# Kernel optimization log

Measured on AMD Instinct MI355X. Metric: run time of the kernel, lower is better.

The kernel has to match this reference:

```python
import jax, jax.numpy as jnp
import numpy as np

B, NQ, NK = 4, 512, 512
DQ, DK, DV = 512, 512, 512
H = 128
MASK_VAL = -1e6


def setup_inputs() -> dict:
    key = jax.random.key(0)
    kq, kk, kv, kwq, kwk, kwv, kl = jax.random.split(key, 7)
    queries = jax.random.normal(kq, (B, NQ, DQ), dtype=jnp.float32)
    keys = jax.random.normal(kk, (B, NK, DK), dtype=jnp.float32)
    values = jax.random.normal(kv, (B, NK, DV), dtype=jnp.float32)
    # Dense(num_hiddens, use_bias=False) weights, Glorot-ish scale
    Wq = jax.random.normal(kwq, (DQ, H), dtype=jnp.float32) / np.sqrt(DQ)
    Wk = jax.random.normal(kwk, (DK, H), dtype=jnp.float32) / np.sqrt(DK)
    Wv = jax.random.normal(kwv, (H,), dtype=jnp.float32) / np.sqrt(H)  # Dense(1) as a vector
    valid_lens = jax.random.randint(kl, (B,), 1, NK + 1, dtype=jnp.int32)
    return {"queries": queries, "keys": keys, "values": values,
            "Wq": Wq, "Wk": Wk, "Wv": Wv, "valid_lens": valid_lens}


def reference(queries, keys, values, Wq, Wk, Wv, valid_lens):
    # Project queries/keys to hidden dim
    q = jnp.einsum('bqd,dh->bqh', queries, Wq)   # [B,NQ,H]
    k = jnp.einsum('bkd,dh->bkh', keys, Wk)      # [B,NK,H]
    # Broadcast add + tanh -> [B,NQ,NK,H] (the big intermediate)
    features = jnp.tanh(q[:, :, None, :] + k[:, None, :, :])
    # W_v reduces hidden dim to a scalar score
    scores = jnp.einsum('bqkh,h->bqk', features, Wv)  # [B,NQ,NK]
    # masked softmax over keys: positions >= valid_len get -1e6 (as in d2l sequence_mask)
    mask = jnp.arange(NK, dtype=jnp.int32)[None, None, :] < valid_lens[:, None, None]
    scores = jnp.where(mask, scores, MASK_VAL)
    attn = jax.nn.softmax(scores, axis=-1)
    # dropout rate 0.0 -> identity
    return jnp.einsum('bqk,bkv->bqv', attn, values)  # [B,NQ,DV]
```

## Files before the change

### kernel.cpp

```cpp
#include <hip/hip_runtime.h>

#ifndef __has_builtin
#define __has_builtin(x) 0
#endif

#if __has_builtin(__builtin_amdgcn_exp2f)
#define EXP2F(x) __builtin_amdgcn_exp2f(x)
#else
#define EXP2F(x) exp2f(x)
#endif
#if __has_builtin(__builtin_amdgcn_rcpf)
#define RCPF(x) __builtin_amdgcn_rcpf(x)
#else
#define RCPF(x) (1.0f / (x))
#endif

static constexpr int NB = 4, NQ = 512, NK = 512, DD = 512, HH = 128, DV = 512;
static constexpr float MASKV = -1e6f;
static constexpr float C2LOG2E = 2.885390081777926814f;

typedef __attribute__((ext_vector_type(8))) short bf16x8;
typedef __attribute__((ext_vector_type(4))) float f32x4;

__device__ __forceinline__ unsigned short f2bf(float x) {
  unsigned int u = __float_as_uint(x);
  u += 0x7FFFu + ((u >> 16) & 1u);
  return (unsigned short)(u >> 16);
}
__device__ __forceinline__ float bf2f(unsigned short h) {
  return __uint_as_float(((unsigned int)h) << 16);
}
__device__ __forceinline__ void split2(float x, unsigned short& hi, unsigned short& lo) {
  hi = f2bf(x);
  lo = f2bf(x - bf2f(hi));
}

__global__ __launch_bounds__(256) void proj_mfma_vt_kernel(
    const float* __restrict__ queries, const float* __restrict__ keys,
    const float* __restrict__ Wq, const float* __restrict__ Wk,
    const float* __restrict__ values, const int* __restrict__ valid_lens,
    float* __restrict__ eq, float* __restrict__ ekT4,
    unsigned short* __restrict__ Vt) {
  __shared__ __align__(16) unsigned short smem_us[20736];
  const int bid = blockIdx.x;
  const int t = threadIdx.x;

  if (bid < 256) {
    const int row0 = bid << 4;
    const bool isK = row0 >= 2048;
    int b = 0, kloc = 0;
    const float* inb;
    const float* W;
    if (isK) {
      const int local = row0 - 2048;
      b = local >> 9;
      kloc = local & 511;
      if (kloc >= valid_lens[b]) return;
      inb = keys + (size_t)local * DD;
      W = Wk;
    } else {
      inb = queries + (size_t)row0 * DD;
      W = Wq;
    }

    unsigned short* Ah = smem_us;
    unsigned short* Al = smem_us + 1152;
    unsigned short* Wh = smem_us + 2304;
    unsigned short* Wl = smem_us + 11520;

    const int w = t >> 6, l = t & 63;
    const int lm = l & 15;
    const int lk8 = (l >> 4) << 3;

    const f32x4 z = {0.f, 0.f, 0.f, 0.f};
    f32x4 acc[2] = {z, z};

    const int ar = t >> 4, ac4 = (t & 15) << 2;
    const int wh = t & 127, wkg = (t >> 7) << 5;

    for (int kt = 0; kt < 8; ++kt) {
      const int k0 = kt << 6;
      {
        const float4 v = *reinterpret_cast<const float4*>(inb + (size_t)ar * DD + k0 + ac4);
        unsigned short h0, h1, h2, h3, l0, l1, l2, l3;
        split2(v.x, h0, l0); split2(v.y, h1, l1);
        split2(v.z, h2, l2); split2(v.w, h3, l3);
        uint2 ph = make_uint2((unsigned int)h0 | ((unsigned int)h1 << 16),
                              (unsigned int)h2 | ((unsigned int)h3 << 16));
        uint2 pl = make_uint2((unsigned int)l0 | ((unsigned int)l1 << 16),
                              (unsigned int)l2 | ((unsigned int)l3 << 16));
        *reinterpret_cast<uint2*>(Ah + ar * 72 + ac4) = ph;
        *reinterpret_cast<uint2*>(Al + ar * 72 + ac4) = pl;
      }
      {
        unsigned int hw[16], lw[16];
#pragma unroll
        for (int i = 0; i < 16; ++i) {
          const float w0 = W[(size_t)(k0 + wkg + 2 * i) * HH + wh];
          const float w1 = W[(size_t)(k0 + wkg + 2 * i + 1) * HH + wh];
          unsigned short a0, a1, b0, b1;
          split2(w0, a0, b0); split2(w1, a1, b1);
          hw[i] = (unsigned int)a0 | ((unsigned int)a1 << 16);
          lw[i] = (unsigned int)b0 | ((unsigned int)b1 << 16);
        }
        unsigned int* dh = reinterpret_cast<unsigned int*>(Wh + wh * 72 + wkg);
        unsigned int* dl = reinterpret_cast<unsigned int*>(Wl + wh * 72 + wkg);
#pragma unroll
        for (int i = 0; i < 4; ++i) {
          *reinterpret_cast<uint4*>(dh + 4 * i) =
              make_uint4(hw[4 * i], hw[4 * i + 1], hw[4 * i + 2], hw[4 * i + 3]);
          *reinterpret_cast<uint4*>(dl + 4 * i) =
              make_uint4(lw[4 * i], lw[4 * i + 1], lw[4 * i + 2], lw[4 * i + 3]);
        }
      }
      __syncthreads();

#pragma unroll
      for (int kh = 0; kh < 2; ++kh) {
        const int ko = lk8 + (kh << 5);
        const bf16x8 ah = *reinterpret_cast<const bf16x8*>(Ah + lm * 72 + ko);
        const bf16x8 al = *reinterpret_cast<const bf16x8*>(Al + lm * 72 + ko);
#pragma unroll
        for (int c = 0; c < 2; ++c) {
          const int hrow = (w << 5) + (c << 4) + lm;
          const bf16x8 bh = *reinterpret_cast<const bf16x8*>(Wh + hrow * 72 + ko);
          const bf16x8 bl = *reinterpret_cast<const bf16x8*>(Wl + hrow * 72 + ko);
          acc[c] = __builtin_amdgcn_mfma_f32_16x16x32_bf16(ah, bh, acc[c], 0, 0, 0);
          acc[c] = __builtin_amdgcn_mfma_f32_16x16x32_bf16(al, bh, acc[c], 0, 0, 0);
          acc[c] = __builtin_amdgcn_mfma_f32_16x16x32_bf16(ah, bl, acc[c], 0, 0, 0);
        }
      }
      __syncthreads();
    }

    const int rb = (l >> 4) << 2;
    if (!isK) {
#pragma unroll
      for (int c = 0; c < 2; ++c) {
        const int h = (w << 5) + (c << 4) + lm;
#pragma unroll
        for (int j = 0; j < 4; ++j)
          eq[(size_t)(row0 + rb + j) * HH + h] = EXP2F(acc[c][j] * C2LOG2E);
      }
    } else {
      float* tile = reinterpret_cast<float*>(smem_us);
#pragma unroll
      for (int c = 0; c < 2; ++c) {
        const int h = (w << 5) + (c << 4) + lm;
#pragma unroll
        for (int j = 0; j < 4; ++j)
          tile[(rb + j) * 132 + h] = EXP2F(acc[c][j] * C2LOG2E);
      }
      __syncthreads();
#pragma unroll
      for (int i = 0; i < 2; ++i) {
        const int idx = t + (i << 8);
        const int k = idx & 15, h4 = idx >> 4;
        const float4 v = *reinterpret_cast<const float4*>(tile + k * 132 + (h4 << 2));
        *reinterpret_cast<float4*>(
            ekT4 + ((((size_t)b * 32 + h4) << 9) + kloc + k) * 4) = v;
      }
    }
  } else {
    unsigned short (*tl)[72] = reinterpret_cast<unsigned short (*)[72]>(smem_us);
    const int vb = bid - 256;
    const int b = vb >> 6;
    const int tile = vb & 63;
    const int k0 = (tile >> 3) << 6;
    const int v0 = (tile & 7) << 6;
    const int kr = t >> 4, c4 = (t & 15) << 2;
#pragma unroll
    for (int pp = 0; pp < 4; ++pp) {
      const int k = kr + (pp << 4);
      const float4 v = *reinterpret_cast<const float4*>(
          values + ((size_t)(b * NK + k0 + k)) * DV + v0 + c4);
      tl[k][c4 + 0] = f2bf(v.x); tl[k][c4 + 1] = f2bf(v.y);
      tl[k][c4 + 2] = f2bf(v.z); tl[k][c4 + 3] = f2bf(v.w);
    }
    __syncthreads();
    const int vr = t >> 2, seg = t & 3;
    unsigned int pk[8];
#pragma unroll
    for (int i = 0; i < 8; ++i) {
      const int kc = (seg << 4) + (i << 1);
      pk[i] = (unsigned int)tl[kc][vr] | ((unsigned int)tl[kc + 1][vr] << 16);
    }
    unsigned short* dst = Vt + ((size_t)(b * NK + v0 + vr)) * NK + k0 + (seg << 4);
    *reinterpret_cast<uint4*>(dst) = make_uint4(pk[0], pk[1], pk[2], pk[3]);
    *reinterpret_cast<uint4*>(dst + 8) = make_uint4(pk[4], pk[5], pk[6], pk[7]);
  }
}

__global__ __launch_bounds__(1024) void scores_softmax_kernel(
    const float* __restrict__ eq, const float* __restrict__ ekT4,
    const float* __restrict__ Wv, const int* __restrict__ valid_lens,
    unsigned short* __restrict__ attnQ) {
  const int b = blockIdx.x >> 7;
  const int q0 = (blockIdx.x & 127) << 2;
  const int t = threadIdx.x;
  const int kk = t & 511, hh = t >> 9;

  __shared__ __align__(16) float qs[4][HH];
  __shared__ __align__(16) float wv[HH];
  __shared__ __align__(16) float scp[2][4][NK];

  if (t < 512) {
    qs[t >> 7][t & 127] = eq[((size_t)(b * NQ + q0 + (t >> 7))) * HH + (t & 127)];
  } else if (t < 640) {
    wv[t - 512] = Wv[t - 512];
  }
  __syncthreads();

  const int vl = valid_lens[b];
  float s0 = 0.f, s1 = 0.f, s2 = 0.f, s3 = 0.f;

  if (kk < vl) {
    const float* ekb4 = ekT4 + (((size_t)(b * 32 + hh * 16) << 9) + kk) * 4;
#pragma unroll 8
    for (int i = 0; i < 16; ++i) {
      const float4 e4 = *reinterpret_cast<const float4*>(ekb4 + ((size_t)i << 11));
      const int h = (hh * 16 + i) << 2;
      const float4 w4 = *reinterpret_cast<const float4*>(&wv[h]);
      const float4 qa = *reinterpret_cast<const float4*>(&qs[0][h]);
      const float4 qb = *reinterpret_cast<const float4*>(&qs[1][h]);
      const float4 qc = *reinterpret_cast<const float4*>(&qs[2][h]);
      const float4 qd = *reinterpret_cast<const float4*>(&qs[3][h]);
      float u, v, num, r;
      u = fmaf(qa.x, e4.x, 1.f); v = fmaf(qa.y, e4.y, 1.f);
      num = fmaf(w4.x, v, w4.y * u); r = RCPF(u * v); s0 = fmaf(num, r, s0);
      u = fmaf(qa.z, e4.z, 1.f); v = fmaf(qa.w, e4.w, 1.f);
      num = fmaf(w4.z, v, w4.w * u); r = RCPF(u * v); s0 = fmaf(num, r, s0);
      u = fmaf(qb.x, e4.x, 1.f); v = fmaf(qb.y, e4.y, 1.f);
      num = fmaf(w4.x, v, w4.y * u); r = RCPF(u * v); s1 = fmaf(num, r, s1);
      u = fmaf(qb.z, e4.z, 1.f); v = fmaf(qb.w, e4.w, 1.f);
      num = fmaf(w4.z, v, w4.w * u); r = RCPF(u * v); s1 = fmaf(num, r, s1);
      u = fmaf(qc.x, e4.x, 1.f); v = fmaf(qc.y, e4.y, 1.f);
      num = fmaf(w4.x, v, w4.y * u); r = RCPF(u * v); s2 = fmaf(num, r, s2);
      u = fmaf(qc.z, e4.z, 1.f); v = fmaf(qc.w, e4.w, 1.f);
      num = fmaf(w4.z, v, w4.w * u); r = RCPF(u * v); s2 = fmaf(num, r, s2);
      u = fmaf(qd.x, e4.x, 1.f); v = fmaf(qd.y, e4.y, 1.f);
      num = fmaf(w4.x, v, w4.y * u); r = RCPF(u * v); s3 = fmaf(num, r, s3);
      u = fmaf(qd.z, e4.z, 1.f); v = fmaf(qd.w, e4.w, 1.f);
      num = fmaf(w4.z, v, w4.w * u); r = RCPF(u * v); s3 = fmaf(num, r, s3);
    }
  }
  scp[hh][0][kk] = s0;
  scp[hh][1][kk] = s1;
  scp[hh][2][kk] = s2;
  scp[hh][3][kk] = s3;
  __syncthreads();

  if (t < 256) {
    const int w = t >> 6, l = t & 63;
    float v[8];
#pragma unroll
    for (int j = 0; j < 8; ++j) {
      const int k = l + (j << 6);
      const float sv = scp[0][w][k] + scp[1][w][k];
      v[j] = (k < vl) ? (-2.f * sv) : MASKV;
    }
    float m = v[0];
#pragma unroll
    for (int j = 1; j < 8; ++j) m = fmaxf(m, v[j]);
#pragma unroll
    for (int off = 32; off > 0; off >>= 1) m = fmaxf(m, __shfl_xor(m, off, 64));
    float p[8], sum = 0.f;
#pragma unroll
    for (int j = 0; j < 8; ++j) {
      p[j] = __expf(v[j] - m);
      sum += p[j];
    }
#pragma unroll
    for (int off = 32; off > 0; off >>= 1) sum += __shfl_xor(sum, off, 64);
    const float inv = RCPF(sum);
#pragma unroll
    for (int j = 0; j < 8; ++j) scp[0][w][l + (j << 6)] = p[j] * inv;
  }
  __syncthreads();

  if (t < 512) {
#pragma unroll
    for (int j = 0; j < 4; ++j)
      attnQ[((size_t)(b * NQ + q0 + j)) * NK + t] = f2bf(scp[0][j][t]);
  }
}

__global__ __launch_bounds__(256) void pv_mfma_kernel(
    const unsigned short* __restrict__ attnQ, const unsigned short* __restrict__ Vt,
    const int* __restrict__ valid_lens, float* __restrict__ out) {
  const int bid = blockIdx.x;
  const int b = (bid & 1) | ((bid >> 8) << 1);
  const int tile = (bid >> 1) & 127;
  const int q0 = (tile >> 4) << 6;
  const int v0 = (tile & 15) << 5;

  __shared__ __align__(16) unsigned short Als[64 * 40];
  __shared__ __align__(16) unsigned short Bls[32 * 40];

  const int t = threadIdx.x;
  const int w = t >> 6, l = t & 63;
  const int lm = l & 15;
  const int lk = (l >> 4) << 3;

  const f32x4 z = {0.f, 0.f, 0.f, 0.f};
  f32x4 acc[2] = {z, z};

  const int vl = valid_lens[b];
  const int nkt = (vl + 31) >> 5;

  const int sq = t >> 2, seg = t & 3;
  const unsigned short* arow = attnQ + ((size_t)(b * NQ + q0 + sq)) * NK;
  unsigned short* alds = &Als[sq * 40 + (seg << 3)];
  const unsigned short* brow = Vt + ((size_t)(b * NK + v0 + (t >> 2))) * NK;
  unsigned short* blds = &Bls[(t >> 2) * 40 + (seg << 3)];

  for (int kt = 0; kt < nkt; ++kt) {
    const int k0 = kt << 5;
    *reinterpret_cast<bf16x8*>(alds) =
        *reinterpret_cast<const bf16x8*>(arow + k0 + (seg << 3));
    if (t < 128)
      *reinterpret_cast<bf16x8*>(blds) =
          *reinterpret_cast<const bf16x8*>(brow + k0 + (seg << 3));
    __syncthreads();

    const bf16x8 af = *reinterpret_cast<const bf16x8*>(
        &Als[((w << 4) + lm) * 40 + lk]);
#pragma unroll
    for (int nv = 0; nv < 2; ++nv) {
      const bf16x8 bfr = *reinterpret_cast<const bf16x8*>(
          &Bls[((nv << 4) + lm) * 40 + lk]);
      acc[nv] = __builtin_amdgcn_mfma_f32_16x16x32_bf16(af, bfr, acc[nv], 0, 0, 0);
    }
    __syncthreads();
  }

  const int rbase = (l >> 4) << 2;
#pragma unroll
  for (int nv = 0; nv < 2; ++nv) {
    const int qg = q0 + (w << 4) + rbase;
    const int vg = v0 + (nv << 4) + lm;
#pragma unroll
    for (int j = 0; j < 4; ++j)
      out[((size_t)(b * NQ + qg + j)) * DV + vg] = acc[nv][j];
  }
}

extern "C" void kernel_launch(void* const* d_in, const int* in_sizes, int n_in,
                              void* d_out, int out_size, void* d_ws, size_t ws_size,
                              hipStream_t stream) {
  (void)in_sizes; (void)n_in; (void)out_size; (void)ws_size;
  const float* queries = (const float*)d_in[0];
  const float* keys    = (const float*)d_in[1];
  const float* values  = (const float*)d_in[2];
  const float* Wq      = (const float*)d_in[3];
  const float* Wk      = (const float*)d_in[4];
  const float* Wv      = (const float*)d_in[5];
  const int*   vlens   = (const int*)d_in[6];
  float* out = (float*)d_out;
  float* ws = (float*)d_ws;

  float* eq   = ws;
  float* ekT4 = ws + 262144;
  unsigned short* attnQ = (unsigned short*)(ws + 524288);
  unsigned short* Vt    = (unsigned short*)(ws + 1048576);

  proj_mfma_vt_kernel<<<512, 256, 0, stream>>>(queries, keys, Wq, Wk, values,
                                               vlens, eq, ekT4, Vt);
  scores_softmax_kernel<<<512, 1024, 0, stream>>>(eq, ekT4, Wv, vlens, attnQ);
  pv_mfma_kernel<<<512, 256, 0, stream>>>(attnQ, Vt, vlens, out);
}
```

Before: 44.87 us.

## Double-buffer PV kernel LDS tiles with larger 64x64 blocks and K=64 steps

Restructures the attention-times-V MFMA kernel so each block computes a 64x64 output tile with 512 threads, 8 waves arranged 4 in q by 2 in v. Each K step now covers 64 instead of 32. A double-buffered LDS scheme prefetches the next K slice into registers while MFMAs run on the current one, which cuts one barrier per iteration. The intent is to hide global load latency and raise data reuse per block. The trade-off is half as many blocks (256), which may reduce occupancy across CUs, and more LDS per block.

```diff
diff --git a/kernel.cpp b/kernel.cpp
--- a/kernel.cpp
+++ b/kernel.cpp
@@ -285,60 +285,84 @@
   }
 }
 
-__global__ __launch_bounds__(256) void pv_mfma_kernel(
+__global__ __launch_bounds__(512) void pv_mfma_kernel(
     const unsigned short* __restrict__ attnQ, const unsigned short* __restrict__ Vt,
     const int* __restrict__ valid_lens, float* __restrict__ out) {
   const int bid = blockIdx.x;
-  const int b = (bid & 1) | ((bid >> 8) << 1);
-  const int tile = (bid >> 1) & 127;
-  const int q0 = (tile >> 4) << 6;
-  const int v0 = (tile & 15) << 5;
-
-  __shared__ __align__(16) unsigned short Als[64 * 40];
-  __shared__ __align__(16) unsigned short Bls[32 * 40];
+  const int b = bid & 3;
+  const int tile = bid >> 2;
+  const int q0 = (tile >> 3) << 6;
+  const int v0 = (tile & 7) << 6;
+
+  __shared__ __align__(16) unsigned short Als[2][64 * 72];
+  __shared__ __align__(16) unsigned short Bls[2][64 * 72];
 
   const int t = threadIdx.x;
   const int w = t >> 6, l = t & 63;
   const int lm = l & 15;
   const int lk = (l >> 4) << 3;
+  const int wq = (w & 3) << 4;
+  const int wv = (w >> 2) << 5;
 
   const f32x4 z = {0.f, 0.f, 0.f, 0.f};
   f32x4 acc[2] = {z, z};
 
   const int vl = valid_lens[b];
-  const int nkt = (vl + 31) >> 5;
-
-  const int sq = t >> 2, seg = t & 3;
-  const unsigned short* arow = attnQ + ((size_t)(b * NQ + q0 + sq)) * NK;
-  unsigned short* alds = &Als[sq * 40 + (seg << 3)];
-  const unsigned short* brow = Vt + ((size_t)(b * NK + v0 + (t >> 2))) * NK;
-  unsigned short* blds = &Bls[(t >> 2) * 40 + (seg << 3)];
+  const int nkt = (vl + 63) >> 6;
+
+  const bool isA = t < 256;
+  const int sr = (t & 255) >> 2, seg = t & 3;
+  const unsigned short* src = isA
+      ? attnQ + ((size_t)(b * NQ + q0 + sr)) * NK + (seg << 3)
+      : Vt + ((size_t)(b * NK + v0 + sr)) * NK + (seg << 3);
+  unsigned short* dst0 = (isA ? Als[0] : Bls[0]) + sr * 72 + (seg << 3);
+  unsigned short* dst1 = (isA ? Als[1] : Bls[1]) + sr * 72 + (seg << 3);
+
+  {
+    const bf16x8 r0 = *reinterpret_cast<const bf16x8*>(src);
+    const bf16x8 r1 = *reinterpret_cast<const bf16x8*>(src + 32);
+    *reinterpret_cast<bf16x8*>(dst0) = r0;
+    *reinterpret_cast<bf16x8*>(dst0 + 32) = r1;
+  }
+  __syncthreads();
 
   for (int kt = 0; kt < nkt; ++kt) {
-    const int k0 = kt << 5;
-    *reinterpret_cast<bf16x8*>(alds) =
-        *reinterpret_cast<const bf16x8*>(arow + k0 + (seg << 3));
-    if (t < 128)
-      *reinterpret_cast<bf16x8*>(blds) =
-          *reinterpret_cast<const bf16x8*>(brow + k0 + (seg << 3));
+    const int cur = kt & 1;
+    const bool more = (kt + 1) < nkt;
+    bf16x8 r0, r1;
+    if (more) {
+      const unsigned short* s = src + (((size_t)(kt + 1)) << 6);
+      r0 = *reinterpret_cast<const bf16x8*>(s);
+      r1 = *reinterpret_cast<const bf16x8*>(s + 32);
+    }
+
+    const unsigned short* Ab = cur ? Als[1] : Als[0];
+    const unsigned short* Bb = cur ? Bls[1] : Bls[0];
+#pragma unroll
+    for (int kh = 0; kh < 2; ++kh) {
+      const int ko = lk + (kh << 5);
+      const bf16x8 af = *reinterpret_cast<const bf16x8*>(Ab + (wq + lm) * 72 + ko);
+#pragma unroll
+      for (int nv = 0; nv < 2; ++nv) {
+        const bf16x8 bfr = *reinterpret_cast<const bf16x8*>(
+            Bb + (wv + (nv << 4) + lm) * 72 + ko);
+        acc[nv] = __builtin_amdgcn_mfma_f32_16x16x32_bf16(af, bfr, acc[nv], 0, 0, 0);
+      }
+    }
+
+    if (more) {
+      unsigned short* d = cur ? dst0 : dst1;
+      *reinterpret_cast<bf16x8*>(d) = r0;
+      *reinterpret_cast<bf16x8*>(d + 32) = r1;
+    }
     __syncthreads();
-
-    const bf16x8 af = *reinterpret_cast<const bf16x8*>(
-        &Als[((w << 4) + lm) * 40 + lk]);
-#pragma unroll
-    for (int nv = 0; nv < 2; ++nv) {
-      const bf16x8 bfr = *reinterpret_cast<const bf16x8*>(
-          &Bls[((nv << 4) + lm) * 40 + lk]);
-      acc[nv] = __builtin_amdgcn_mfma_f32_16x16x32_bf16(af, bfr, acc[nv], 0, 0, 0);
-    }
-    __syncthreads();
   }
 
   const int rbase = (l >> 4) << 2;
 #pragma unroll
   for (int nv = 0; nv < 2; ++nv) {
-    const int qg = q0 + (w << 4) + rbase;
-    const int vg = v0 + (nv << 4) + lm;
+    const int qg = q0 + wq + rbase;
+    const int vg = v0 + wv + (nv << 4) + lm;
 #pragma unroll
     for (int j = 0; j < 4; ++j)
       out[((size_t)(b * NQ + qg + j)) * DV + vg] = acc[nv][j];
@@ -367,5 +391,5 @@
   proj_mfma_vt_kernel<<<512, 256, 0, stream>>>(queries, keys, Wq, Wk, values,
                                                vlens, eq, ekT4, Vt);
   scores_softmax_kernel<<<512, 1024, 0, stream>>>(eq, ekT4, Wv, vlens, attnQ);
-  pv_mfma_kernel<<<512, 256, 0, stream>>>(attnQ, Vt, vlens, out);
-}
+  pv_mfma_kernel<<<256, 512, 0, stream>>>(attnQ, Vt, vlens, out);
+}
```

Result: faster. 40.10 us (-10.6%).
